# Kernel tuning notes

Hardware: AMD Instinct MI355X
Metric: run time of the kernel (lower is better)

The kernel has to match this reference:

```python
import jax, jax.numpy as jnp
import numpy as np

# Hyperparameters matching init_kwargs / repo defaults
MARGIN = 0.2
ALPHA = 0.1          # opt.alpha
OT_ITER = 20         # opt.OT_iteration
BETA = 0.5           # IPOT temperature (hardcoded in repo's OT module)
SIM_TYPE = "MISA"    # opt.sim_type_dot
MAX_VIOLATION = True
EPS = 1e-12

N_IMAGE = 128
N_REG = 36
D = 1024
MAX_WORD = 60


def _matchmap_sim(M):
    # M: (n_image, n_regions, n_word)
    if SIM_TYPE == "SISA":
        return M.mean(axis=2).mean(axis=1)
    elif SIM_TYPE == "MISA":
        return M.max(axis=1).mean(axis=1)
    elif SIM_TYPE == "SIMA":
        return M.max(axis=2).mean(axis=1)
    raise ValueError


def _ipot_distance(C, n, m):
    # C: (bs, n, m) cosine-distance cost; IPOT with uniform marginals.
    bs = C.shape[0]
    # Torch code detaches T, so no gradient flows through the iteration.
    A = jnp.exp(-jax.lax.stop_gradient(C) / BETA)

    def body(_, carry):
        T, sigma = carry
        Q = A * T                                            # (bs, n, m)
        delta = 1.0 / (n * jnp.matmul(Q, sigma))             # (bs, n, 1)
        sigma = 1.0 / (m * jnp.matmul(Q.transpose(0, 2, 1), delta))  # (bs, m, 1)
        T = delta * Q * sigma.transpose(0, 2, 1)
        return (T, sigma)

    T0 = jnp.ones((bs, n, m), C.dtype)
    s0 = jnp.ones((bs, m, 1), C.dtype) / m
    T, _ = jax.lax.fori_loop(0, OT_ITER, body, (T0, s0))
    T = jax.lax.stop_gradient(T)
    # batch_trace(C^T T) == sum(C * T) per batch element
    return -jnp.sum(C * T, axis=(1, 2))                      # (bs,)


def _scores(im, s, cap_lens):
    n_reg = im.shape[1]
    imn = im / (jnp.linalg.norm(im, axis=2, keepdims=True) + EPS)
    lens = np.asarray(cap_lens)
    sims, sims_ot = [], []
    for i in range(s.shape[0]):  # ragged per-caption loop (as in original)
        n_word = int(lens[i])
        cap = s[i, :n_word, :]                               # (w, d)
        # matchmap: bmm(images, cap^T) -> (n_image, n_regions, n_word)
        M = jnp.einsum('brd,wd->brw', im, cap)
        sims.append(_matchmap_sim(M))
        capn = cap / (jnp.linalg.norm(cap, axis=1, keepdims=True) + EPS)
        # cost_matrix_batch_torch(cap^T, img^T).transpose -> (n_image, n_reg, n_word)
        C = 1.0 - jnp.einsum('brd,wd->brw', imn, capn)
        sims_ot.append(_ipot_distance(C, n_reg, n_word))
    return jnp.stack(sims, axis=1), jnp.stack(sims_ot, axis=1)  # (n_img, n_cap)


def _loss(im, s, cap_lens):
    scores, scores_ot = _scores(im, s, cap_lens)
    n = scores.shape[0]
    eye = jnp.eye(n, dtype=bool)

    def costs(sc):
        d = jnp.diag(sc)[:, None]                            # (n, 1)
        cs = jnp.clip(MARGIN + sc - d, 0.0)                  # caption-side
        ci = jnp.clip(MARGIN + sc - d.T, 0.0)                # image-side
        cs = jnp.where(eye, 0.0, cs)
        ci = jnp.where(eye, 0.0, ci)
        return cs, ci

    cost_s, cost_im = costs(scores)
    cost_s_ot, cost_im_ot = costs(scores_ot)
    cost_s = cost_s + ALPHA * cost_s_ot
    cost_im = cost_im + ALPHA * cost_im_ot
    if MAX_VIOLATION:
        cost_s = cost_s.max(axis=1)
        cost_im = cost_im.max(axis=0)
        cost_s_ot = cost_s_ot.max(axis=1)
        cost_im_ot = cost_im_ot.max(axis=0)
    return (cost_s.sum() + cost_im.sum(), cost_s_ot.sum() + cost_im_ot.sum())


def setup_inputs() -> dict:
    key = jax.random.key(0)
    k1, k2, k3 = jax.random.split(key, 3)
    im = jax.random.normal(k1, (N_IMAGE, N_REG, D), dtype=jnp.float32)
    s = jax.random.normal(k2, (N_IMAGE, MAX_WORD, D), dtype=jnp.float32)
    rng = np.random.default_rng(0)
    s_l = np.asarray(rng.integers(10, MAX_WORD + 1, size=N_IMAGE), dtype=np.int64)
    x = jax.random.normal(k3, (1,), dtype=jnp.float32)  # unused by forward math
    return {"im": im, "s": s, "s_l": s_l, "x": x}


def reference(im, s, s_l, x):
    return _loss(im, s, s_l)
```

## Files before the change

kernel.cpp:

```cpp
#include <hip/hip_runtime.h>
#include <hip/hip_bf16.h>
#include <math.h>

#define N_IMAGE 128
#define N_REG   36
#define DIM     1024
#define MAX_WORD 60
#define OT_ITERS 20
#define MARGIN_F 0.2f
#define ALPHA_F  0.1f
#define EPS_F    1e-12f

#define APAN  16384
#define AIMG  (3 * APAN)
#define BCAP  (4 * APAN)

typedef short bf16x8 __attribute__((ext_vector_type(8)));
typedef float f32x4  __attribute__((ext_vector_type(4)));
typedef float f32x2  __attribute__((ext_vector_type(2)));
typedef unsigned int u32x2 __attribute__((ext_vector_type(2)));

#if defined(__has_builtin)
#if __has_builtin(__builtin_amdgcn_permlane16_swap) && __has_builtin(__builtin_amdgcn_permlane32_swap)
#define HAVE_PL_SWAP 1
#endif
#endif


__device__ __forceinline__ unsigned int pkbf2(float a, float b) {
    union { __hip_bfloat162 h2; unsigned int u; } cv;
    cv.h2 = __float22bfloat162_rn(make_float2(a, b));
    return cv.u;
}
__device__ __forceinline__ float lo16(unsigned int u) { return __int_as_float((int)(u << 16)); }
__device__ __forceinline__ float hi16(unsigned int u) { return __int_as_float((int)(u & 0xFFFF0000u)); }

#define SWZ(x, pat) __int_as_float(__builtin_amdgcn_ds_swizzle(__float_as_int(x), (pat)))
#define BPERM(a, x) __int_as_float(__builtin_amdgcn_ds_bpermute((a), __float_as_int(x)))
#define DPPADD(x, ctrl) \
    ((x) + __int_as_float(__builtin_amdgcn_update_dpp(0, __float_as_int(x), (ctrl), 0xf, 0xf, true)))

__device__ __forceinline__ float bfly16_sum(float x) {
    x = DPPADD(x, 0xB1);
    x = DPPADD(x, 0x4E);
    x = DPPADD(x, 0x124);
    x = DPPADD(x, 0x128);
    return x;
}

__device__ __forceinline__ float xq_sum(float x) {
#ifdef HAVE_PL_SWAP
    u32x2 p = __builtin_amdgcn_permlane16_swap(
        (unsigned)__float_as_int(x), (unsigned)__float_as_int(x), false, false);
    const float s = __int_as_float((int)p.x) + __int_as_float((int)p.y);
    u32x2 r = __builtin_amdgcn_permlane32_swap(
        (unsigned)__float_as_int(s), (unsigned)__float_as_int(s), false, false);
    return __int_as_float((int)r.x) + __int_as_float((int)r.y);
#else
    x += SWZ(x, 0x401F);
    const int xaddr = (((int)(threadIdx.x & 63) ^ 32) << 2);
    x += BPERM(xaddr, x);
    return x;
#endif
}
__device__ __forceinline__ float xq_max(float x) {
#ifdef HAVE_PL_SWAP
    u32x2 p = __builtin_amdgcn_permlane16_swap(
        (unsigned)__float_as_int(x), (unsigned)__float_as_int(x), false, false);
    const float s = fmaxf(__int_as_float((int)p.x), __int_as_float((int)p.y));
    u32x2 r = __builtin_amdgcn_permlane32_swap(
        (unsigned)__float_as_int(s), (unsigned)__float_as_int(s), false, false);
    return fmaxf(__int_as_float((int)r.x), __int_as_float((int)r.y));
#else
    x = fmaxf(x, SWZ(x, 0x401F));
    const int xaddr = (((int)(threadIdx.x & 63) ^ 32) << 2);
    x = fmaxf(x, BPERM(xaddr, x));
    return x;
#endif
}
__device__ __forceinline__ float bfly64_sum(float x) {
    return xq_sum(bfly16_sum(x));
}


__global__ __launch_bounds__(256) void pack_kernel(
    const float* __restrict__ im, const float* __restrict__ s,
    float* __restrict__ inv_im, float* __restrict__ inv_cap,
    float* __restrict__ out,
    unsigned short* __restrict__ imp, unsigned short* __restrict__ sp) {

    const int pid = blockIdx.x;
    const int tid = threadIdx.x;
    if (pid == 0 && tid == 0) { out[0] = 0.0f; out[1] = 0.0f; }

    const int w = tid >> 6, lane = tid & 63, q = lane >> 4, l15 = lane & 15;
    const bool isim = (pid < 384);
    int obj, p, nvalid;
    const float* src;
    unsigned short* dst;
    if (isim) {
        obj = pid / 3; p = pid % 3;
        src = im + (size_t)obj * 36 * DIM;
        dst = imp + (size_t)obj * AIMG + (size_t)p * APAN;
        nvalid = 36;
    } else {
        const int k = pid - 384;
        obj = k >> 2; p = k & 3;
        src = s + (size_t)obj * 60 * DIM;
        dst = sp + (size_t)obj * BCAP + (size_t)p * APAN;
        nvalid = 60;
    }
    const int row = p * 16 + l15;
    const bool valid = (row < nvalid);

    float ss = 0.0f;
    #pragma unroll
    for (int i = 0; i < 4; ++i) {
        const int c = w * 4 + i;
        #pragma unroll
        for (int h = 0; h < 2; ++h) {
            float4 v0 = make_float4(0.f, 0.f, 0.f, 0.f), v1 = v0;
            if (valid) {
                const float* rp = src + (size_t)row * DIM + c * 64 + h * 32 + q * 8;
                v0 = *(const float4*)rp;
                v1 = *(const float4*)(rp + 4);
            }
            ss += v0.x * v0.x + v0.y * v0.y + v0.z * v0.z + v0.w * v0.w
                + v1.x * v1.x + v1.y * v1.y + v1.z * v1.z + v1.w * v1.w;
            uint4 o;
            o.x = pkbf2(v0.x, v0.y); o.y = pkbf2(v0.z, v0.w);
            o.z = pkbf2(v1.x, v1.y); o.w = pkbf2(v1.z, v1.w);
            *(uint4*)(dst + (size_t)c * 1024 + h * 512 + q * 128 + l15 * 8) = o;
        }
    }
    ss = xq_sum(ss);
    __shared__ float sh[4][16];
    if (lane < 16) sh[w][lane] = ss;
    __syncthreads();
    if (tid < 16) {
        const float t = sh[0][tid] + sh[1][tid] + sh[2][tid] + sh[3][tid];
        const int r = p * 16 + tid;
        if (r < nvalid) {
            const float inv = 1.0f / (sqrtf(t) + EPS_F);
            if (isim) inv_im[obj * 36 + r] = inv;
            else      inv_cap[obj * 60 + r] = inv;
        }
    }
}


__global__ void norms_kernel(const float* __restrict__ im, const float* __restrict__ s,
                             float* __restrict__ inv_im, float* __restrict__ inv_cap,
                             float* __restrict__ out) {
    if (blockIdx.x == 0 && threadIdx.x == 0) { out[0] = 0.0f; out[1] = 0.0f; }
    const int NIM = N_IMAGE * N_REG;
    const int NS  = N_IMAGE * MAX_WORD;
    int row  = blockIdx.x * 4 + (threadIdx.x >> 6);
    int lane = threadIdx.x & 63;
    if (row >= NIM + NS) return;
    const bool isim = (row < NIM);
    const float* base = isim ? (im + (size_t)row * DIM)
                             : (s  + (size_t)(row - NIM) * DIM);
    const float4* b4 = (const float4*)base;
    float acc = 0.0f;
    for (int k = lane; k < DIM / 4; k += 64) {
        float4 v = b4[k];
        acc += v.x * v.x + v.y * v.y + v.z * v.z + v.w * v.w;
    }
    for (int off = 32; off; off >>= 1) acc += __shfl_down(acc, off, 64);
    if (lane == 0) {
        float inv = 1.0f / (sqrtf(acc) + EPS_F);
        if (isim) inv_im[row] = inv;
        else      inv_cap[row - NIM] = inv;
    }
}


template <int CT>
__device__ __forceinline__ void ot_epilogue(
    f32x4 (&acc)[3 * CT], const float* invImS, const float* invCapS,
    int cap, int b0, int m, float* __restrict__ S, float* __restrict__ SOT) {

    const int tid  = threadIdx.x;
    const int lane = tid & 63;
    const int wv   = tid >> 6;
    const int q    = lane >> 4;
    const int l15  = lane & 15;
    const float mf    = (float)m;
    const float inv_m = 1.0f / mf;

    constexpr int PK = (CT + 1) / 2;
    float icap[CT]; bool vw[CT];
    #pragma unroll
    for (int ct = 0; ct < CT; ++ct) {
        const int w = ct * 16 + l15;
        vw[ct]   = (w < m);
        icap[ct] = (w < 60) ? invCapS[w] : 0.0f;
    }

    unsigned int apk[12][PK];
    float mxv[CT];
    #pragma unroll
    for (int ct = 0; ct < CT; ++ct) mxv[ct] = -3e38f;

    #pragma unroll
    for (int j = 0; j < 12; ++j) {
        const int rt = j >> 2, p = j & 3;
        const int r  = rt * 16 + q * 4 + p;
        const bool rowok = (rt < 2) || (q == 0);
        const float iir = rowok ? invImS[wv * 36 + (r < 36 ? r : 0)] : 0.0f;
        float av[CT];
        #pragma unroll
        for (int ct = 0; ct < CT; ++ct) {
            const float Mv = acc[rt * CT + ct][p];
            mxv[ct] = fmaxf(mxv[ct], rowok ? Mv : -3e38f);
            const float cv = 1.0f - Mv * iir * icap[ct];
            const bool ok  = rowok && vw[ct];
            av[ct] = ok ? __expf(-2.0f * cv) : 0.0f;
        }
        #pragma unroll
        for (int pk = 0; pk < PK; ++pk)
            apk[j][pk] = pkbf2(av[2 * pk], (2 * pk + 1 < CT) ? av[2 * pk + 1] : 0.0f);
    }

    {
        const int baddr = l15 << 2;
        #pragma unroll
        for (int pk = 0; pk < PK; ++pk) {
            const int r0 = __builtin_amdgcn_ds_bpermute(baddr, (int)apk[8][pk]);
            const int r1 = __builtin_amdgcn_ds_bpermute(baddr, (int)apk[9][pk]);
            const int r2 = __builtin_amdgcn_ds_bpermute(baddr, (int)apk[10][pk]);
            const int r3 = __builtin_amdgcn_ds_bpermute(baddr, (int)apk[11][pk]);
            const int lo = (q & 1) ? r1 : r0;
            const int hi = (q & 1) ? r3 : r2;
            apk[8][pk] = (unsigned int)((q & 2) ? hi : lo);
        }
    }

    f32x2 af[9][PK];
    #pragma unroll
    for (int j = 0; j < 9; ++j)
        #pragma unroll
        for (int pk = 0; pk < PK; ++pk) {
            af[j][pk].x = lo16(apk[j][pk]);
            af[j][pk].y = hi16(apk[j][pk]);
        }

    const int b = b0 + wv;
    {
        float sp = 0.0f;
        #pragma unroll
        for (int ct = 0; ct < CT; ++ct) {
            float v = xq_max(mxv[ct]);
            sp += vw[ct] ? v : 0.0f;
        }
        sp = bfly64_sum(sp);
        if (lane == 0) S[(size_t)b * N_IMAGE + cap] = sp * inv_m * 0.25f;
    }

    f32x2 t2[9][PK];
    f32x2 sig2[PK];
    #pragma unroll
    for (int pk = 0; pk < PK; ++pk) {
        const bool v0 = vw[2 * pk];
        const bool v1 = (2 * pk + 1 < CT) && vw[2 * pk + 1];
        sig2[pk].x = v0 ? inv_m : 0.0f;
        sig2[pk].y = v1 ? inv_m : 0.0f;
        #pragma unroll
        for (int j = 0; j < 9; ++j) {
            t2[j][pk].x = v0 ? mf : 0.0f;
            t2[j][pk].y = v1 ? mf : 0.0f;
        }
    }

    for (int it = 0; it < OT_ITERS; ++it) {
        f32x2 s2[PK], csum[PK];
        #pragma unroll
        for (int pk = 0; pk < PK; ++pk) {
            s2[pk]   = sig2[pk] * sig2[pk];
            csum[pk] = (f32x2){0.0f, 0.0f};
        }
        #pragma unroll
        for (int j = 0; j < 9; ++j) {
            f32x2 at[PK];
            #pragma unroll
            for (int pk = 0; pk < PK; ++pk)
                at[pk] = af[j][pk] * t2[j][pk];
            f32x2 u2 = at[0] * s2[0];
            #pragma unroll
            for (int pk = 1; pk < PK; ++pk) u2 += at[pk] * s2[pk];
            const float R  = bfly16_sum(u2.x + u2.y);
            const float dl = __builtin_amdgcn_rcpf(36.0f * R);
            f32x2 dl2; dl2.x = dl; dl2.y = dl;
            #pragma unroll
            for (int pk = 0; pk < PK; ++pk) {
                const f32x2 tn = at[pk] * (dl2 * sig2[pk]);
                t2[j][pk] = tn;
                csum[pk] += tn;
            }
        }
        #pragma unroll
        for (int pk = 0; pk < PK; ++pk) {
            const float cx = xq_sum(csum[pk].x);
            const float cy = xq_sum(csum[pk].y);
            const bool v0 = vw[2 * pk];
            const bool v1 = (2 * pk + 1 < CT) && vw[2 * pk + 1];
            sig2[pk].x = v0 ? __builtin_amdgcn_rcpf(mf * cx) : 0.0f;
            sig2[pk].y = v1 ? __builtin_amdgcn_rcpf(mf * cy) : 0.0f;
        }
    }

    {
        float pp = 0.0f;
        #pragma unroll
        for (int j = 0; j < 9; ++j) {
            #pragma unroll
            for (int pk = 0; pk < PK; ++pk) {
                const float cvx = -0.5f * __logf(fmaxf(af[j][pk].x, 1e-30f));
                pp = fmaf(cvx, t2[j][pk].x * sig2[pk].x, pp);
                if (2 * pk + 1 < CT) {
                    const float cvy = -0.5f * __logf(fmaxf(af[j][pk].y, 1e-30f));
                    pp = fmaf(cvy, t2[j][pk].y * sig2[pk].y, pp);
                }
            }
        }
        pp = bfly64_sum(pp);
        if (lane == 0) SOT[(size_t)b * N_IMAGE + cap] = -pp;
    }
}


template <int CT>
__device__ __forceinline__ void pair_body_fast(
    const unsigned short* __restrict__ imp, const unsigned short* __restrict__ sp,
    const float* invImS, const float* invCapS,
    int cap, int b0, int m,
    float* __restrict__ S, float* __restrict__ SOT) {

    const int tid  = threadIdx.x;
    const int lane = tid & 63;
    const int wv   = tid >> 6;
    const int q    = lane >> 4;
    const int l15  = lane & 15;

    const unsigned short* Ab = imp + (size_t)(b0 + wv) * AIMG + (q * 128 + l15 * 8);
    const unsigned short* Bb = sp  + (size_t)cap * BCAP        + (q * 128 + l15 * 8);

    f32x4 acc[3 * CT];
    #pragma unroll
    for (int t = 0; t < 3 * CT; ++t) acc[t] = (f32x4){0.f, 0.f, 0.f, 0.f};

    bf16x8 a0[3], bf0[CT], a1[3], bf1[CT];
    #pragma unroll
    for (int rt = 0; rt < 3; ++rt) a0[rt] = *(const bf16x8*)(Ab + rt * APAN);
    #pragma unroll
    for (int ct = 0; ct < CT; ++ct) bf0[ct] = *(const bf16x8*)(Bb + ct * APAN);

    #pragma unroll 1
    for (int c = 0; c < 16; ++c) {
        const unsigned short* Ac = Ab + c * 1024;
        const unsigned short* Bc = Bb + c * 1024;
        #pragma unroll
        for (int rt = 0; rt < 3; ++rt) a1[rt] = *(const bf16x8*)(Ac + rt * APAN + 512);
        #pragma unroll
        for (int ct = 0; ct < CT; ++ct) bf1[ct] = *(const bf16x8*)(Bc + ct * APAN + 512);
        #pragma unroll
        for (int rt = 0; rt < 3; ++rt)
            #pragma unroll
            for (int ct = 0; ct < CT; ++ct)
                acc[rt * CT + ct] = __builtin_amdgcn_mfma_f32_16x16x32_bf16(
                    a0[rt], bf0[ct], acc[rt * CT + ct], 0, 0, 0);
        const int cn = (c < 15) ? c + 1 : 15;
        const unsigned short* An = Ab + cn * 1024;
        const unsigned short* Bn = Bb + cn * 1024;
        #pragma unroll
        for (int rt = 0; rt < 3; ++rt) a0[rt] = *(const bf16x8*)(An + rt * APAN);
        #pragma unroll
        for (int ct = 0; ct < CT; ++ct) bf0[ct] = *(const bf16x8*)(Bn + ct * APAN);
        #pragma unroll
        for (int rt = 0; rt < 3; ++rt)
            #pragma unroll
            for (int ct = 0; ct < CT; ++ct)
                acc[rt * CT + ct] = __builtin_amdgcn_mfma_f32_16x16x32_bf16(
                    a1[rt], bf1[ct], acc[rt * CT + ct], 0, 0, 0);
    }

    __syncthreads();
    ot_epilogue<CT>(acc, invImS, invCapS, cap, b0, m, S, SOT);
}

__global__ __launch_bounds__(256, 4)
void pair_fast(const unsigned short* __restrict__ imp,
               const unsigned short* __restrict__ sp,
               const int* __restrict__ s_l,
               const float* __restrict__ inv_im, const float* __restrict__ inv_cap,
               float* __restrict__ S, float* __restrict__ SOT) {
    const int cap = blockIdx.x;
    const int b0  = blockIdx.y * 4;
    const int tid = threadIdx.x;

    __shared__ float invImS[144];
    __shared__ float invCapS[60];
    if (tid < 144) invImS[tid] = inv_im[b0 * 36 + tid];
    else if (tid < 204) invCapS[tid - 144] = inv_cap[cap * 60 + (tid - 144)];

    const int m  = s_l[cap];
    const int CT = __builtin_amdgcn_readfirstlane((m + 15) >> 4);
    switch (CT) {
    case 1: pair_body_fast<1>(imp, sp, invImS, invCapS, cap, b0, m, S, SOT); break;
    case 2: pair_body_fast<2>(imp, sp, invImS, invCapS, cap, b0, m, S, SOT); break;
    case 3: pair_body_fast<3>(imp, sp, invImS, invCapS, cap, b0, m, S, SOT); break;
    default: pair_body_fast<4>(imp, sp, invImS, invCapS, cap, b0, m, S, SOT); break;
    }
}


template <int CT>
__device__ __forceinline__ void pair_body_slow(
    const float* __restrict__ im, const float* __restrict__ s,
    char* smem, const float* invImS, const float* invCapS,
    int cap, int b0, int m,
    float* __restrict__ S, float* __restrict__ SOT) {

    const int tid  = threadIdx.x;
    const int lane = tid & 63;
    const int wv   = tid >> 6;
    const int q    = lane >> 4;
    const int l15  = lane & 15;
    const int q4   = tid & 15;
    const int row0 = tid >> 4;

    const char* sA = smem;
    const char* sB = smem + 27648;

    f32x4 acc[3 * CT];
    #pragma unroll
    for (int t = 0; t < 3 * CT; ++t) acc[t] = (f32x4){0.f, 0.f, 0.f, 0.f};

    for (int c = 0; c < 16; ++c) {
        const int col = c * 64 + q4 * 4;
        #pragma unroll
        for (int img = 0; img < 4; ++img) {
            #pragma unroll
            for (int j = 0; j < 3; ++j) {
                const int r = row0 + 16 * j;
                if (j < 2 || row0 < 4) {
                    const size_t ro = (size_t)(b0 * 36 + img * 36 + r) * 1024 + col;
                    float4 v = *(const float4*)(im + ro);
                    uint2 w2; w2.x = pkbf2(v.x, v.y); w2.y = pkbf2(v.z, v.w);
                    *(uint2*)(smem + (img * 48 + r) * 144 + q4 * 8) = w2;
                }
            }
        }
        #pragma unroll
        for (int j = 0; j < CT; ++j) {
            const int r = row0 + 16 * j;
            if (CT < 4 || j < 3 || row0 < 12) {
                const size_t ro = (size_t)(cap * 60 + r) * 1024 + col;
                float4 v = *(const float4*)(s + ro);
                uint2 w2; w2.x = pkbf2(v.x, v.y); w2.y = pkbf2(v.z, v.w);
                *(uint2*)(smem + (192 + r) * 144 + q4 * 8) = w2;
            }
        }
        __syncthreads();
        #pragma unroll
        for (int h = 0; h < 2; ++h) {
            bf16x8 bfr[CT];
            #pragma unroll
            for (int ct = 0; ct < CT; ++ct)
                bfr[ct] = *(const bf16x8*)(sB + (ct * 16 + l15) * 144 + h * 64 + q * 16);
            #pragma unroll
            for (int rt = 0; rt < 3; ++rt) {
                bf16x8 afr = *(const bf16x8*)(sA + (wv * 48 + rt * 16 + l15) * 144 + h * 64 + q * 16);
                #pragma unroll
                for (int ct = 0; ct < CT; ++ct)
                    acc[rt * CT + ct] = __builtin_amdgcn_mfma_f32_16x16x32_bf16(
                        afr, bfr[ct], acc[rt * CT + ct], 0, 0, 0);
            }
        }
        __syncthreads();
    }
    ot_epilogue<CT>(acc, invImS, invCapS, cap, b0, m, S, SOT);
}

__global__ __launch_bounds__(256, 4)
void pair_slow(const float* __restrict__ im, const float* __restrict__ s,
               const int* __restrict__ s_l,
               const float* __restrict__ inv_im, const float* __restrict__ inv_cap,
               float* __restrict__ S, float* __restrict__ SOT) {
    const int cap = blockIdx.x;
    const int b0  = blockIdx.y * 4;
    const int tid = threadIdx.x;

    __shared__ __align__(16) char smem[36864];
    __shared__ float invImS[144];
    __shared__ float invCapS[60];

    if (tid < 144) invImS[tid] = inv_im[b0 * 36 + tid];
    else if (tid < 204) invCapS[tid - 144] = inv_cap[cap * 60 + (tid - 144)];

    const int m = s_l[cap];
    {
        float4 z = make_float4(0.f, 0.f, 0.f, 0.f);
        #pragma unroll
        for (int j = 0; j < 9; ++j)
            *(float4*)(smem + (tid + j * 256) * 16) = z;
    }
    __syncthreads();

    const int CT = __builtin_amdgcn_readfirstlane((m + 15) >> 4);
    switch (CT) {
    case 1: pair_body_slow<1>(im, s, smem, invImS, invCapS, cap, b0, m, S, SOT); break;
    case 2: pair_body_slow<2>(im, s, smem, invImS, invCapS, cap, b0, m, S, SOT); break;
    case 3: pair_body_slow<3>(im, s, smem, invImS, invCapS, cap, b0, m, S, SOT); break;
    default: pair_body_slow<4>(im, s, smem, invImS, invCapS, cap, b0, m, S, SOT); break;
    }
}


__global__ void loss_kernel(const float* __restrict__ S, const float* __restrict__ SOT,
                            float* __restrict__ out) {
    const int j = blockIdx.x;
    const int t = threadIdx.x;
    __shared__ float sh[4][2];
    const float db  = S[j * 129];
    const float dob = SOT[j * 129];
    float rv = 0.f, rov = 0.f, cv = 0.f, cov = 0.f;
    if (t != j) {
        float cs  = fmaxf(0.0f, MARGIN_F + S[j * 128 + t] - db);
        float cso = fmaxf(0.0f, MARGIN_F + SOT[j * 128 + t] - dob);
        rv = cs + ALPHA_F * cso;  rov = cso;
        float ci  = fmaxf(0.0f, MARGIN_F + S[t * 128 + j] - db);
        float cio = fmaxf(0.0f, MARGIN_F + SOT[t * 128 + j] - dob);
        cv = ci + ALPHA_F * cio;  cov = cio;
    }
    for (int off = 32; off; off >>= 1) {
        rv  = fmaxf(rv,  __shfl_down(rv,  off, 64));
        rov = fmaxf(rov, __shfl_down(rov, off, 64));
        cv  = fmaxf(cv,  __shfl_down(cv,  off, 64));
        cov = fmaxf(cov, __shfl_down(cov, off, 64));
    }
    if ((t & 63) == 0) {
        sh[0][t >> 6] = rv; sh[1][t >> 6] = rov;
        sh[2][t >> 6] = cv; sh[3][t >> 6] = cov;
    }
    __syncthreads();
    if (t == 0) {
        float a0 = fmaxf(sh[0][0], sh[0][1]) + fmaxf(sh[2][0], sh[2][1]);
        float a1 = fmaxf(sh[1][0], sh[1][1]) + fmaxf(sh[3][0], sh[3][1]);
        atomicAdd(&out[0], a0);
        atomicAdd(&out[1], a1);
    }
}

extern "C" void kernel_launch(void* const* d_in, const int* in_sizes, int n_in,
                              void* d_out, int out_size, void* d_ws, size_t ws_size,
                              hipStream_t stream) {
    const float* im  = (const float*)d_in[0];
    const float* s   = (const float*)d_in[1];
    const int*   s_l = (const int*)d_in[2];
    float* out = (float*)d_out;
    float* ws  = (float*)d_ws;

    float* inv_im  = ws;
    float* inv_cap = ws + 4608;
    float* S       = ws + 12288;
    float* SOT     = ws + 12288 + 16384;
    unsigned short* imp = (unsigned short*)((char*)d_ws + 180224);
    unsigned short* sp  = imp + (size_t)N_IMAGE * AIMG;
    const size_t need = 180224 +
        ((size_t)N_IMAGE * AIMG + (size_t)N_IMAGE * BCAP) * 2;
    const int fast = (ws_size >= need) ? 1 : 0;

    if (fast) {
        pack_kernel<<<dim3(896), dim3(256), 0, stream>>>(
            im, s, inv_im, inv_cap, out, imp, sp);
        pair_fast<<<dim3(N_IMAGE, N_IMAGE / 4), dim3(256), 0, stream>>>(
            imp, sp, s_l, inv_im, inv_cap, S, SOT);
    } else {
        norms_kernel<<<dim3((4608 + 7680) / 4), dim3(256), 0, stream>>>(
            im, s, inv_im, inv_cap, out);
        pair_slow<<<dim3(N_IMAGE, N_IMAGE / 4), dim3(256), 0, stream>>>(
            im, s, s_l, inv_im, inv_cap, S, SOT);
    }
    loss_kernel<<<dim3(N_IMAGE), dim3(128), 0, stream>>>(S, SOT, out);
}
```

Before: 293.2 us.

## Split fused GEMM+OT kernel into separate GEMM and OT kernels via workspace

Splits the fused pair kernel into a GEMM kernel that computes the matchmap, MISA score and packed bf16 exp(-C/beta) tiles into a global buffer, and a separate OT kernel that loads those tiles and runs the IPOT iterations. The aim is to let each kernel use registers and occupancy suited to its phase instead of one kernel holding both GEMM accumulators and OT state. In exchange it writes and reads about 75 MB of intermediate data and adds a launch. The split path runs only when the workspace is large enough; otherwise it falls back to the fused path.

```diff
diff --git a/kernel.cpp b/kernel.cpp
--- a/kernel.cpp
+++ b/kernel.cpp
@@ -14,6 +14,7 @@
 #define APAN  16384
 #define AIMG  (3 * APAN)
 #define BCAP  (4 * APAN)
+#define AOT   1152
 
 typedef short bf16x8 __attribute__((ext_vector_type(8)));
 typedef float f32x4  __attribute__((ext_vector_type(4)));
@@ -177,29 +178,19 @@
 
 
 template <int CT>
-__device__ __forceinline__ void ot_epilogue(
+__device__ __forceinline__ void build_apk(
     f32x4 (&acc)[3 * CT], const float* invImS, const float* invCapS,
-    int cap, int b0, int m, float* __restrict__ S, float* __restrict__ SOT) {
-
-    const int tid  = threadIdx.x;
-    const int lane = tid & 63;
-    const int wv   = tid >> 6;
-    const int q    = lane >> 4;
-    const int l15  = lane & 15;
-    const float mf    = (float)m;
-    const float inv_m = 1.0f / mf;
+    int m, int wv, int q, int l15,
+    unsigned int (*apk)[(CT + 1) / 2], float* mxv, bool* vw) {
 
     constexpr int PK = (CT + 1) / 2;
-    float icap[CT]; bool vw[CT];
+    float icap[CT];
     #pragma unroll
     for (int ct = 0; ct < CT; ++ct) {
         const int w = ct * 16 + l15;
         vw[ct]   = (w < m);
         icap[ct] = (w < 60) ? invCapS[w] : 0.0f;
     }
-
-    unsigned int apk[12][PK];
-    float mxv[CT];
     #pragma unroll
     for (int ct = 0; ct < CT; ++ct) mxv[ct] = -3e38f;
 
@@ -236,28 +227,14 @@
             apk[8][pk] = (unsigned int)((q & 2) ? hi : lo);
         }
     }
-
-    f32x2 af[9][PK];
-    #pragma unroll
-    for (int j = 0; j < 9; ++j)
-        #pragma unroll
-        for (int pk = 0; pk < PK; ++pk) {
-            af[j][pk].x = lo16(apk[j][pk]);
-            af[j][pk].y = hi16(apk[j][pk]);
-        }
-
-    const int b = b0 + wv;
-    {
-        float sp = 0.0f;
-        #pragma unroll
-        for (int ct = 0; ct < CT; ++ct) {
-            float v = xq_max(mxv[ct]);
-            sp += vw[ct] ? v : 0.0f;
-        }
-        sp = bfly64_sum(sp);
-        if (lane == 0) S[(size_t)b * N_IMAGE + cap] = sp * inv_m * 0.25f;
-    }
-
+}
+
+
+template <int CT>
+__device__ __forceinline__ float ot_iterate(
+    f32x2 (*af)[(CT + 1) / 2], const bool* vw, float mf, float inv_m) {
+
+    constexpr int PK = (CT + 1) / 2;
     f32x2 t2[9][PK];
     f32x2 sig2[PK];
     #pragma unroll
@@ -310,43 +287,46 @@
         }
     }
 
-    {
-        float pp = 0.0f;
-        #pragma unroll
-        for (int j = 0; j < 9; ++j) {
-            #pragma unroll
-            for (int pk = 0; pk < PK; ++pk) {
-                const float cvx = -0.5f * __logf(fmaxf(af[j][pk].x, 1e-30f));
-                pp = fmaf(cvx, t2[j][pk].x * sig2[pk].x, pp);
-                if (2 * pk + 1 < CT) {
-                    const float cvy = -0.5f * __logf(fmaxf(af[j][pk].y, 1e-30f));
-                    pp = fmaf(cvy, t2[j][pk].y * sig2[pk].y, pp);
-                }
+    float pp = 0.0f;
+    #pragma unroll
+    for (int j = 0; j < 9; ++j) {
+        #pragma unroll
+        for (int pk = 0; pk < PK; ++pk) {
+            const float cvx = -0.5f * __logf(fmaxf(af[j][pk].x, 1e-30f));
+            pp = fmaf(cvx, t2[j][pk].x * sig2[pk].x, pp);
+            if (2 * pk + 1 < CT) {
+                const float cvy = -0.5f * __logf(fmaxf(af[j][pk].y, 1e-30f));
+                pp = fmaf(cvy, t2[j][pk].y * sig2[pk].y, pp);
             }
         }
-        pp = bfly64_sum(pp);
-        if (lane == 0) SOT[(size_t)b * N_IMAGE + cap] = -pp;
-    }
+    }
+    return bfly64_sum(pp);
 }
 
 
 template <int CT>
-__device__ __forceinline__ void pair_body_fast(
+__device__ __forceinline__ void misa_write(
+    const float* mxv, const bool* vw, float inv_m, int lane,
+    float* __restrict__ S, int b, int cap) {
+    float sp = 0.0f;
+    #pragma unroll
+    for (int ct = 0; ct < CT; ++ct) {
+        float v = xq_max(mxv[ct]);
+        sp += vw[ct] ? v : 0.0f;
+    }
+    sp = bfly64_sum(sp);
+    if (lane == 0) S[(size_t)b * N_IMAGE + cap] = sp * inv_m * 0.25f;
+}
+
+
+template <int CT>
+__device__ __forceinline__ void gemm_core(
     const unsigned short* __restrict__ imp, const unsigned short* __restrict__ sp,
-    const float* invImS, const float* invCapS,
-    int cap, int b0, int m,
-    float* __restrict__ S, float* __restrict__ SOT) {
-
-    const int tid  = threadIdx.x;
-    const int lane = tid & 63;
-    const int wv   = tid >> 6;
-    const int q    = lane >> 4;
-    const int l15  = lane & 15;
+    int cap, int b0, int wv, int q, int l15, f32x4 (&acc)[3 * CT]) {
 
     const unsigned short* Ab = imp + (size_t)(b0 + wv) * AIMG + (q * 128 + l15 * 8);
     const unsigned short* Bb = sp  + (size_t)cap * BCAP        + (q * 128 + l15 * 8);
 
-    f32x4 acc[3 * CT];
     #pragma unroll
     for (int t = 0; t < 3 * CT; ++t) acc[t] = (f32x4){0.f, 0.f, 0.f, 0.f};
 
@@ -384,9 +364,165 @@
                 acc[rt * CT + ct] = __builtin_amdgcn_mfma_f32_16x16x32_bf16(
                     a1[rt], bf1[ct], acc[rt * CT + ct], 0, 0, 0);
     }
+}
+
+
+template <int CT>
+__device__ __forceinline__ void gemm_body(
+    const unsigned short* __restrict__ imp, const unsigned short* __restrict__ sp,
+    const float* invImS, const float* invCapS,
+    int cap, int b0, int m,
+    float* __restrict__ S, unsigned int* __restrict__ gA) {
+
+    const int tid  = threadIdx.x;
+    const int lane = tid & 63;
+    const int wv   = tid >> 6;
+    const int q    = lane >> 4;
+    const int l15  = lane & 15;
+    constexpr int PK = (CT + 1) / 2;
+
+    f32x4 acc[3 * CT];
+    gemm_core<CT>(imp, sp, cap, b0, wv, q, l15, acc);
 
     __syncthreads();
-    ot_epilogue<CT>(acc, invImS, invCapS, cap, b0, m, S, SOT);
+
+    unsigned int apk[12][PK];
+    float mxv[CT]; bool vw[CT];
+    build_apk<CT>(acc, invImS, invCapS, m, wv, q, l15, apk, mxv, vw);
+
+    const int b = b0 + wv;
+    misa_write<CT>(mxv, vw, 1.0f / (float)m, lane, S, b, cap);
+
+    unsigned int* dst = gA + (size_t)(b * N_IMAGE + cap) * AOT;
+    if (PK == 1) {
+        #pragma unroll
+        for (int j = 0; j < 9; ++j) dst[j * 128 + lane] = apk[j][0];
+    } else {
+        #pragma unroll
+        for (int j = 0; j < 9; ++j) {
+            uint2 v; v.x = apk[j][0]; v.y = apk[j][1];
+            *(uint2*)(dst + j * 128 + lane * 2) = v;
+        }
+    }
+}
+
+__global__ __launch_bounds__(256, 4)
+void gemm_kernel(const unsigned short* __restrict__ imp,
+                 const unsigned short* __restrict__ sp,
+                 const int* __restrict__ s_l,
+                 const float* __restrict__ inv_im, const float* __restrict__ inv_cap,
+                 float* __restrict__ S, unsigned int* __restrict__ gA) {
+    const int cap = blockIdx.x;
+    const int b0  = blockIdx.y * 4;
+    const int tid = threadIdx.x;
+
+    __shared__ float invImS[144];
+    __shared__ float invCapS[60];
+    if (tid < 144) invImS[tid] = inv_im[b0 * 36 + tid];
+    else if (tid < 204) invCapS[tid - 144] = inv_cap[cap * 60 + (tid - 144)];
+
+    const int m  = s_l[cap];
+    const int CT = __builtin_amdgcn_readfirstlane((m + 15) >> 4);
+    switch (CT) {
+    case 1: gemm_body<1>(imp, sp, invImS, invCapS, cap, b0, m, S, gA); break;
+    case 2: gemm_body<2>(imp, sp, invImS, invCapS, cap, b0, m, S, gA); break;
+    case 3: gemm_body<3>(imp, sp, invImS, invCapS, cap, b0, m, S, gA); break;
+    default: gemm_body<4>(imp, sp, invImS, invCapS, cap, b0, m, S, gA); break;
+    }
+}
+
+
+template <int CT>
+__device__ __forceinline__ void ot_body(
+    const unsigned int* __restrict__ gA, int cap, int b0, int m,
+    float* __restrict__ SOT) {
+
+    const int tid  = threadIdx.x;
+    const int lane = tid & 63;
+    const int wv   = tid >> 6;
+    const int l15  = lane & 15;
+    const float mf    = (float)m;
+    const float inv_m = 1.0f / mf;
+    constexpr int PK = (CT + 1) / 2;
+
+    bool vw[CT];
+    #pragma unroll
+    for (int ct = 0; ct < CT; ++ct) vw[ct] = (ct * 16 + l15) < m;
+
+    const int b = b0 + wv;
+    const unsigned int* src = gA + (size_t)(b * N_IMAGE + cap) * AOT;
+
+    f32x2 af[9][PK];
+    #pragma unroll
+    for (int j = 0; j < 9; ++j) {
+        if (PK == 1) {
+            const unsigned int u = src[j * 128 + lane];
+            af[j][0].x = lo16(u); af[j][0].y = hi16(u);
+        } else {
+            const uint2 v = *(const uint2*)(src + j * 128 + lane * 2);
+            af[j][0].x = lo16(v.x); af[j][0].y = hi16(v.x);
+            af[j][1].x = lo16(v.y); af[j][1].y = hi16(v.y);
+        }
+    }
+
+    const float pp = ot_iterate<CT>(af, vw, mf, inv_m);
+    if (lane == 0) SOT[(size_t)b * N_IMAGE + cap] = -pp;
+}
+
+__global__ __launch_bounds__(256, 4)
+void ot_kernel(const unsigned int* __restrict__ gA, const int* __restrict__ s_l,
+               float* __restrict__ SOT) {
+    const int cap = blockIdx.x;
+    const int b0  = blockIdx.y * 4;
+    const int m   = s_l[cap];
+    const int CT  = __builtin_amdgcn_readfirstlane((m + 15) >> 4);
+    switch (CT) {
+    case 1: ot_body<1>(gA, cap, b0, m, SOT); break;
+    case 2: ot_body<2>(gA, cap, b0, m, SOT); break;
+    case 3: ot_body<3>(gA, cap, b0, m, SOT); break;
+    default: ot_body<4>(gA, cap, b0, m, SOT); break;
+    }
+}
+
+
+template <int CT>
+__device__ __forceinline__ void pair_body_fast(
+    const unsigned short* __restrict__ imp, const unsigned short* __restrict__ sp,
+    const float* invImS, const float* invCapS,
+    int cap, int b0, int m,
+    float* __restrict__ S, float* __restrict__ SOT) {
+
+    const int tid  = threadIdx.x;
+    const int lane = tid & 63;
+    const int wv   = tid >> 6;
+    const int q    = lane >> 4;
+    const int l15  = lane & 15;
+    const float mf    = (float)m;
+    const float inv_m = 1.0f / mf;
+    constexpr int PK = (CT + 1) / 2;
+
+    f32x4 acc[3 * CT];
+    gemm_core<CT>(imp, sp, cap, b0, wv, q, l15, acc);
+
+    __syncthreads();
+
+    unsigned int apk[12][PK];
+    float mxv[CT]; bool vw[CT];
+    build_apk<CT>(acc, invImS, invCapS, m, wv, q, l15, apk, mxv, vw);
+
+    f32x2 af[9][PK];
+    #pragma unroll
+    for (int j = 0; j < 9; ++j)
+        #pragma unroll
+        for (int pk = 0; pk < PK; ++pk) {
+            af[j][pk].x = lo16(apk[j][pk]);
+            af[j][pk].y = hi16(apk[j][pk]);
+        }
+
+    const int b = b0 + wv;
+    misa_write<CT>(mxv, vw, inv_m, lane, S, b, cap);
+    const float pp = ot_iterate<CT>(af, vw, mf, inv_m);
+    if (lane == 0) SOT[(size_t)b * N_IMAGE + cap] = -pp;
 }
 
 __global__ __launch_bounds__(256, 4)
@@ -429,6 +565,9 @@
     const int l15  = lane & 15;
     const int q4   = tid & 15;
     const int row0 = tid >> 4;
+    const float mf    = (float)m;
+    const float inv_m = 1.0f / mf;
+    constexpr int PK = (CT + 1) / 2;
 
     const char* sA = smem;
     const char* sB = smem + 27648;
@@ -480,7 +619,24 @@
         }
         __syncthreads();
     }
-    ot_epilogue<CT>(acc, invImS, invCapS, cap, b0, m, S, SOT);
+
+    unsigned int apk[12][PK];
+    float mxv[CT]; bool vw[CT];
+    build_apk<CT>(acc, invImS, invCapS, m, wv, q, l15, apk, mxv, vw);
+
+    f32x2 af[9][PK];
+    #pragma unroll
+    for (int j = 0; j < 9; ++j)
+        #pragma unroll
+        for (int pk = 0; pk < PK; ++pk) {
+            af[j][pk].x = lo16(apk[j][pk]);
+            af[j][pk].y = hi16(apk[j][pk]);
+        }
+
+    const int b = b0 + wv;
+    misa_write<CT>(mxv, vw, inv_m, lane, S, b, cap);
+    const float pp = ot_iterate<CT>(af, vw, mf, inv_m);
+    if (lane == 0) SOT[(size_t)b * N_IMAGE + cap] = -pp;
 }
 
 __global__ __launch_bounds__(256, 4)
@@ -565,14 +721,24 @@
     float* inv_im  = ws;
     float* inv_cap = ws + 4608;
     float* S       = ws + 12288;
-    float* SOT     = ws + 12288 + 16384;
+    float* SOT     = ws + 28672;
     unsigned short* imp = (unsigned short*)((char*)d_ws + 180224);
     unsigned short* sp  = imp + (size_t)N_IMAGE * AIMG;
-    const size_t need = 180224 +
+    unsigned int*   gA  = (unsigned int*)(sp + (size_t)N_IMAGE * BCAP);
+
+    const size_t need_fast  = 180224 +
         ((size_t)N_IMAGE * AIMG + (size_t)N_IMAGE * BCAP) * 2;
-    const int fast = (ws_size >= need) ? 1 : 0;
-
-    if (fast) {
+    const size_t need_split = need_fast +
+        (size_t)N_IMAGE * N_IMAGE * AOT * 4;
+
+    if (ws_size >= need_split) {
+        pack_kernel<<<dim3(896), dim3(256), 0, stream>>>(
+            im, s, inv_im, inv_cap, out, imp, sp);
+        gemm_kernel<<<dim3(N_IMAGE, N_IMAGE / 4), dim3(256), 0, stream>>>(
+            imp, sp, s_l, inv_im, inv_cap, S, gA);
+        ot_kernel<<<dim3(N_IMAGE, N_IMAGE / 4), dim3(256), 0, stream>>>(
+            gA, s_l, SOT);
+    } else if (ws_size >= need_fast) {
         pack_kernel<<<dim3(896), dim3(256), 0, stream>>>(
             im, s, inv_im, inv_cap, out, imp, sp);
         pair_fast<<<dim3(N_IMAGE, N_IMAGE / 4), dim3(256), 0, stream>>>(
```

After: 347.0 us. 18.4% more time.
